# Performance work log

Hardware: AMD Instinct MI355X
Metric: run time of the kernel (lower is better)

The kernel has to match this reference:

```python
import jax, jax.numpy as jnp
import numpy as np

SCALE = 256.0  # emulates SharedFxpShift = 8 fixed-point shift


def requant(x):
    # RequantFxpToScaledInt8: shift down by SharedFxpShift and clamp to int8 range
    return jnp.clip(x / SCALE, -128.0, 127.0)


def prelu(x, a):
    return jnp.where(x >= 0, x, a * x)


def _linearize(c):
    # injective encoding of 3D int coords (coords in [-8, 2040) after +8 shift)
    c = c.astype(jnp.int64) + 8
    B = 2048
    return (c[:, 0] * B + c[:, 1]) * B + c[:, 2]


def sparse_conv(coords, feats, W, stride):
    # 3x3x3 submanifold sparse conv: for each kernel offset, hash-lookup the
    # neighbor via sorted linearized coords + searchsorted, gather, matmul.
    # coords [N,3] int32, feats [N,Cin], W [27,Cin,Cout]
    lin = _linearize(coords)
    perm = jnp.argsort(lin)
    slin = lin[perm]
    N = coords.shape[0]
    out = jnp.zeros((N, W.shape[-1]), feats.dtype)
    k = 0
    for dx in (-1, 0, 1):
        for dy in (-1, 0, 1):
            for dz in (-1, 0, 1):
                off = jnp.array([dx, dy, dz], jnp.int32) * stride
                q = _linearize(coords + off[None, :])
                pos = jnp.clip(jnp.searchsorted(slin, q), 0, N - 1)
                hit = slin[pos] == q
                nb = perm[pos]
                f = jnp.where(hit[:, None], feats[nb], 0.0)
                out = out + f @ W[k]
                k += 1
    return out


def setup_inputs() -> dict:
    N, M, C = 200000, 400000, 64
    rng = np.random.default_rng(0)
    # unique parent coords: multiples of 2 in 512^3 grid
    lin = rng.choice(2 ** 24, size=N, replace=False).astype(np.int64)
    px = (lin // (256 * 256)) % 256
    py = (lin // 256) % 256
    pz = lin % 256
    rec_C = (np.stack([px, py, pz], 1) * 2).astype(np.int32)  # [N,3], stride 2
    # exactly M occupied children out of N*8, sorted (row-major mask order)
    child_idx = np.sort(rng.choice(N * 8, size=M, replace=False)).astype(np.int32)
    parent = child_idx // 8
    bit = child_idx % 8
    off = np.stack([(bit >> 2) & 1, (bit >> 1) & 1, bit & 1], 1).astype(np.int32)
    child_C = rec_C[parent] + off  # [M,3], stride 1, unique
    bins1_bits = np.zeros((N, 8), np.int32)
    bins1_bits[parent, bit] = 1
    bins0_bits = rng.integers(0, 2, size=(M, 8)).astype(np.int32)

    key = jax.random.key(0)
    ks = jax.random.split(key, 20)

    def w(k, shape, fan_in):
        return jax.random.normal(k, shape, jnp.float32) / np.sqrt(fan_in)

    inp = {
        "rec_F": jax.random.normal(ks[0], (N, C), jnp.float32) * SCALE,
        "dec_W": w(ks[1], (C + 8, C), C + 8),
        "dec_b": w(ks[2], (C,), 1) * 0.1,
        "dec_a": jnp.full((C,), 0.25, jnp.float32),
        "res_W1": w(ks[3], (27, C, C), 27 * C),
        "res_b1": w(ks[4], (C,), 1) * 0.1,
        "res_a1": jnp.full((C,), 0.25, jnp.float32),
        "res_W2": w(ks[5], (27, C, C), 27 * C),
        "res_b2": w(ks[6], (C,), 1) * 0.1,
        "p0_Wc": w(ks[7], (27, C, C), 27 * C),
        "p0_bc": w(ks[8], (C,), 1) * 0.1,
        "p0_ac": jnp.full((C,), 0.25, jnp.float32),
        "p0_Wl": w(ks[9], (C, C * 8), C),
        "p1_Wc": w(ks[10], (27, C, C), 27 * C),
        "p1_bc": w(ks[11], (C,), 1) * 0.1,
        "p1_ac": jnp.full((C,), 0.25, jnp.float32),
        "p1_Wl": w(ks[12], (C, 255), C),
        "rec_C": jnp.asarray(rec_C),
        "bins1_bits": jnp.asarray(bins1_bits),
        "child_idx": jnp.asarray(child_idx),
        "child_C": jnp.asarray(child_C),
        "bins0_bits": jnp.asarray(bins0_bits),
    }
    return inp


def reference(rec_F, dec_W, dec_b, dec_a, res_W1, res_b1, res_a1, res_W2, res_b2,
              p0_Wc, p0_bc, p0_ac, p0_Wl, p1_Wc, p1_bc, p1_ac, p1_Wl,
              rec_C, bins1_bits, child_idx, child_C, bins0_bits):
    C = dec_W.shape[1]
    # embed (empty Sequential for pred_steps=2): bins1.F << SharedFxpShift
    embed_f = bins1_bits.astype(jnp.float32) * SCALE  # [N,8]
    x = jnp.concatenate([rec_F, embed_f], 1)  # [N, C+8]
    # dec: Requant -> LinearPReLU(C+8 -> C, out32) -> ResBlock(C)
    h = requant(x)
    h = prelu(h @ dec_W + dec_b, dec_a)  # [N,C]
    r = requant(h)
    r = prelu(sparse_conv(rec_C, r, res_W1, 2) + res_b1, res_a1)
    r = requant(r)
    r = sparse_conv(rec_C, r, res_W2, 2) + res_b2
    rec_out = h + r  # [N,C]
    # pred[0]: Requant -> SparseConvPReLU(out8) -> Linear(C -> 8C, out32)
    p = requant(rec_out)
    p = requant(prelu(sparse_conv(rec_C, p, p0_Wc, 2) + p0_bc, p0_ac))
    p = p @ p0_Wl  # [N, 8C]
    # boolean-mask gather of occupied children: reshape [N,8,C] then mask ->
    # equals flat row gather with precomputed sorted child indices
    p = p.reshape(-1, C)[child_idx]  # [M,C]
    # pred[1] (last): Requant -> SparseConvPReLU(out8) -> Linear(C -> 255, out32)
    p = requant(p)
    p = requant(prelu(sparse_conv(child_C, p, p1_Wc, 1) + p1_bc, p1_ac))
    pred_out = p @ p1_Wl  # [M,255]
    # cur_oct = (cur_bins[0].F << bin2oct_kernel).sum(1) - 1
    k = jnp.arange(8, dtype=jnp.int32)
    cur_oct = ((bins0_bits << k).sum(1) - 1).astype(jnp.int16)  # [M]
    return rec_out, pred_out, cur_oct
```

## Files before the change

### kernel.cpp

```cpp
#include <hip/hip_runtime.h>
#include <stdint.h>


typedef short bf16x8 __attribute__((ext_vector_type(8)));
typedef float f32x4 __attribute__((ext_vector_type(4)));

#define EMPTY_KEY 0xFFFFFFFFu

__device__ __forceinline__ float rq(float x) {
  x *= (1.0f / 256.0f);
  return fminf(fmaxf(x, -128.0f), 127.0f);
}

__device__ __forceinline__ short f2b(float f) {
  union { float f; uint32_t u; } v; v.f = f;
  uint32_t u = v.u;
  uint32_t r = (u + 0x7FFFu + ((u >> 16) & 1u)) >> 16;
  return (short)r;
}

__device__ __forceinline__ uint32_t hkey(int x, int y, int z) {
  return ((uint32_t)(x + 8) << 20) | ((uint32_t)(y + 8) << 10) | (uint32_t)(z + 8);
}
__device__ __forceinline__ uint32_t hfun(uint32_t key, uint32_t mask) {
  return (key * 2654435761u) & mask;
}


__device__ __forceinline__ void pack_conv_elem(const float* __restrict__ W,
                                               short* __restrict__ dst, int gid) {
  int lane = gid & 63;
  int c = (gid >> 6) & 3;
  int t = (gid >> 8) & 1;
  int k = gid >> 9;
  int n = c * 16 + (lane & 15);
  int g = lane >> 4;
  bf16x8 v;
#pragma unroll
  for (int e = 0; e < 8; e++) {
    int kk = t * 32 + g * 8 + e;
    v[e] = f2b(W[(k * 64 + kk) * 64 + n]);
  }
  *(bf16x8*)(dst + gid * 8) = v;
}

__device__ __forceinline__ void pack_dense_elem(const float* __restrict__ W,
                                                short* __restrict__ dst, int K,
                                                int Ncols, int KT, int CT, int gid) {
  if (gid >= KT * CT * 64) return;
  int lane = gid & 63;
  int c = (gid >> 6) % CT;
  int t = gid / (64 * CT);
  int n = c * 16 + (lane & 15);
  int g = lane >> 4;
  bf16x8 v;
#pragma unroll
  for (int e = 0; e < 8; e++) {
    int kk = t * 32 + g * 8 + e;
    float val = (kk < K && n < Ncols) ? W[kk * Ncols + n] : 0.0f;
    v[e] = f2b(val);
  }
  *(bf16x8*)(dst + gid * 8) = v;
}

struct SetupA {
  const float *dec_W, *p0_Wl, *p1_Wl, *res_W1, *res_W2, *p0_Wc, *p1_Wc;
  const int *bins1, *child_idx, *bins0;
  uint32_t* rkeys;
  short *wpack, *decwp, *p0wp, *p1wp;
  int *bitsPk, *pStart, *bcnt;
  float* outOct;
  int N, M;
};

__global__ void __launch_bounds__(256) k_setupA(SetupA s) {
  int bid = blockIdx.x, tid = threadIdx.x;
  if (bid < 2048) {
    s.rkeys[bid * 256 + tid] = EMPTY_KEY;
    return;
  }
  bid -= 2048;
  if (bid < 216) {
    int which = bid / 54, sb = bid % 54;
    int gid = sb * 256 + tid;
    if (gid < 27 * 2 * 4 * 64) {
      const float* W = which == 0 ? s.res_W1 : which == 1 ? s.res_W2
                     : which == 2 ? s.p0_Wc : s.p1_Wc;
      pack_conv_elem(W, s.wpack + which * 110592, gid);
    }
    return;
  }
  bid -= 216;
  if (bid < 27) {
    if (bid < 3) pack_dense_elem(s.dec_W, s.decwp, 72, 64, 3, 4, bid * 256 + tid);
    else if (bid < 19) pack_dense_elem(s.p0_Wl, s.p0wp, 64, 512, 2, 32, (bid - 3) * 256 + tid);
    else pack_dense_elem(s.p1_Wl, s.p1wp, 64, 255, 2, 16, (bid - 19) * 256 + tid);
    return;
  }
  bid -= 27;
  int nbN = (s.N + 255) / 256, nbM = (s.M + 255) / 256;
  if (bid < nbN) {
    int p = bid * 256 + tid;
    if (p < s.N) {
      int b = 0;
#pragma unroll
      for (int e = 0; e < 8; e++) b |= (s.bins1[(size_t)p * 8 + e] & 1) << e;
      s.bitsPk[p] = b;
    }
    return;
  }
  bid -= nbN;
  if (bid < nbM) {
    int m = bid * 256 + tid;
    if (m < s.M) {
      int p = s.child_idx[m] >> 3;
      if (m == 0 || (s.child_idx[m - 1] >> 3) != p) s.pStart[p] = m;
    }
    return;
  }
  bid -= nbM;
  if (bid < nbM) {
    int m = bid * 256 + tid;
    if (m < s.M) {
      int ss = 0;
#pragma unroll
      for (int e = 0; e < 8; e++) ss += s.bins0[(size_t)m * 8 + e] << e;
      s.outOct[m] = (float)(ss - 1);
    }
    return;
  }
  if (tid < 8) s.bcnt[tid] = 0;
}

__global__ void __launch_bounds__(256)
k_setupB(const int* __restrict__ rec_C, const int* __restrict__ child_idx,
         uint32_t* __restrict__ rkeys, int* __restrict__ rvals,
         int* __restrict__ lists, int* __restrict__ cnt, int N, int M) {
  int bid = blockIdx.x, tid = threadIdx.x;
  int nbN = (N + 255) / 256;
  if (bid < nbN) {
    int i = bid * 256 + tid;
    if (i >= N) return;
    uint32_t key = hkey(rec_C[i * 3], rec_C[i * 3 + 1], rec_C[i * 3 + 2]);
    uint32_t s = hfun(key, (1u << 19) - 1);
    while (true) {
      uint32_t old = atomicCAS(&rkeys[s], EMPTY_KEY, key);
      if (old == EMPTY_KEY) { rvals[s] = i; return; }
      s = (s + 1) & ((1u << 19) - 1);
    }
  }
  bid -= nbN;
  __shared__ int lcnt[8];
  __shared__ int lbase[8];
  if (tid < 8) lcnt[tid] = 0;
  __syncthreads();
  int m = bid * 256 + tid;
  int b = 0, lp = 0;
  if (m < M) {
    b = child_idx[m] & 7;
    lp = atomicAdd(&lcnt[b], 1);
  }
  __syncthreads();
  if (tid < 8) lbase[tid] = atomicAdd(&cnt[tid], lcnt[tid]);
  __syncthreads();
  if (m < M) lists[(size_t)b * M + lbase[b] + lp] = m;
}

__global__ void __launch_bounds__(256)
k_setupC1(const int* __restrict__ rec_C,
          const uint32_t* __restrict__ rkeys, const int* __restrict__ rvals,
          int* __restrict__ nbrR, int N) {
  const uint32_t rmask = (1u << 19) - 1;
  int t = blockIdx.x * 256 + threadIdx.x;
  if (t >= N * 27) return;
  int i = t / 27, k = t % 27;
  int dx = k / 9 - 1, dy = (k / 3) % 3 - 1, dz = k % 3 - 1;
  int x = rec_C[i * 3] + dx * 2;
  int y = rec_C[i * 3 + 1] + dy * 2;
  int z = rec_C[i * 3 + 2] + dz * 2;
  uint32_t key = hkey(x, y, z);
  uint32_t s = hfun(key, rmask);
  int res = -1;
  while (true) {
    uint32_t kk = rkeys[s];
    if (kk == key) { res = rvals[s]; break; }
    if (kk == EMPTY_KEY) break;
    s = (s + 1) & rmask;
  }
  nbrR[(size_t)i * 28 + k] = res;
}

__global__ void __launch_bounds__(256)
k_setupC2(const int* __restrict__ child_C, const int* __restrict__ child_idx,
          const int* __restrict__ nbrR, const int* __restrict__ bitsPacked,
          const int* __restrict__ parentStart, int* __restrict__ nbrC, int M) {
  int m = blockIdx.x * 256 + threadIdx.x;
  if (m >= M) return;
  int cx = child_C[(size_t)m * 3], cy = child_C[(size_t)m * 3 + 1],
      cz = child_C[(size_t)m * 3 + 2];
  int pr = child_idx[m] >> 3;
  const int* nrow = nbrR + (size_t)pr * 28;
  int px = cx & 1, py = cy & 1, pz = cz & 1;

  int b8[8], s8[8];
#pragma unroll
  for (int j = 0; j < 8; j++) {
    int ddx = (px - 1) + ((j >> 2) & 1);
    int ddy = (py - 1) + ((j >> 1) & 1);
    int ddz = (pz - 1) + (j & 1);
    int kk = (ddx + 1) * 9 + (ddy + 1) * 3 + (ddz + 1);
    int r = nrow[kk];
    b8[j] = (r >= 0) ? bitsPacked[r] : 0;
    s8[j] = (r >= 0) ? parentStart[r] : 0;
  }

  int nout[28];
  nout[27] = -1;
#pragma unroll
  for (int k = 0; k < 27; k++) {
    const int dx = k / 9 - 1, dy = (k / 3) % 3 - 1, dz = k % 3 - 1;
    int tx = cx + dx, ty = cy + dy, tz = cz + dz;
    int jx = ((px + dx + 2) >> 1) - px;
    int jy = ((py + dy + 2) >> 1) - py;
    int jz = ((pz + dz + 2) >> 1) - pz;
    int j = jx * 4 + jy * 2 + jz;
    int bit = ((tx & 1) << 2) | ((ty & 1) << 1) | (tz & 1);
    int bits = b8[j];
    int res = -1;
    if ((bits >> bit) & 1) res = s8[j] + __popc(bits & ((1 << bit) - 1));
    nout[k] = res;
  }
#pragma unroll
  for (int q = 0; q < 7; q++)
    *(int4*)(nbrC + (size_t)m * 28 + q * 4) =
        make_int4(nout[q * 4], nout[q * 4 + 1], nout[q * 4 + 2], nout[q * 4 + 3]);
}


__global__ void __launch_bounds__(256)
k_dec(const float* __restrict__ recF, const int* __restrict__ bits,
      const short* __restrict__ wp, const float* __restrict__ bias,
      const float* __restrict__ alpha, float* __restrict__ h32,
      short* __restrict__ hq) {
  int tid = threadIdx.x, wid = tid >> 6, lane = tid & 63;
  int rowbase = blockIdx.x * 64 + wid * 16;
  int lrow = rowbase + (lane & 15);
  int g = lane >> 4;
  f32x4 acc[4] = {};
#pragma unroll
  for (int t = 0; t < 3; t++) {
    bf16x8 a = {0, 0, 0, 0, 0, 0, 0, 0};
    if (t < 2) {
      const float* src = recF + (size_t)lrow * 64 + t * 32 + g * 8;
#pragma unroll
      for (int e = 0; e < 8; e++) a[e] = f2b(rq(src[e]));
    } else if (g == 0) {
      const int* bp = bits + (size_t)lrow * 8;
#pragma unroll
      for (int e = 0; e < 8; e++) a[e] = f2b((float)bp[e]);
    }
#pragma unroll
    for (int c = 0; c < 4; c++) {
      bf16x8 b = *(const bf16x8*)(wp + ((t * 4 + c) * 64 + lane) * 8);
      acc[c] = __builtin_amdgcn_mfma_f32_16x16x32_bf16(a, b, acc[c], 0, 0, 0);
    }
  }
#pragma unroll
  for (int c = 0; c < 4; c++) {
    int col = c * 16 + (lane & 15);
    float bi = bias[col], al = alpha[col];
#pragma unroll
    for (int r = 0; r < 4; r++) {
      int row = rowbase + g * 4 + r;
      float v = acc[c][r] + bi;
      v = v >= 0.0f ? v : al * v;
      h32[(size_t)row * 64 + col] = v;
      hq[(size_t)row * 64 + col] = f2b(rq(v));
    }
  }
}

template <int MODE>
__global__ void __launch_bounds__(256)
k_conv(const short* __restrict__ fin, const int* __restrict__ nbr,
       const short* __restrict__ wp, const float* __restrict__ bias,
       const float* __restrict__ alpha, const float* __restrict__ resid,
       float* __restrict__ out32, short* __restrict__ outq) {
  int tid = threadIdx.x, wid = tid >> 6, lane = tid & 63;
  int rowbase = blockIdx.x * 64 + wid * 16;
  int lrow = rowbase + (lane & 15);
  int g = lane >> 4;

  int4 nv[7];
#pragma unroll
  for (int j = 0; j < 7; j++)
    nv[j] = *(const int4*)(nbr + (size_t)lrow * 28 + j * 4);
  int nbk[28];
#pragma unroll
  for (int j = 0; j < 7; j++) {
    nbk[j * 4 + 0] = nv[j].x;
    nbk[j * 4 + 1] = nv[j].y;
    nbk[j * 4 + 2] = nv[j].z;
    nbk[j * 4 + 3] = nv[j].w;
  }

  const bf16x8 zz = {0, 0, 0, 0, 0, 0, 0, 0};
  f32x4 acc[4] = {};
#pragma unroll
  for (int k = 0; k < 27; k++) {
    if (__any(nbk[k] >= 0)) {
      int nb = nbk[k];
      int safe = nb >= 0 ? nb : 0;
      const short* fp = fin + (size_t)safe * 64 + g * 8;
      bf16x8 a0 = *(const bf16x8*)fp;
      bf16x8 a1 = *(const bf16x8*)(fp + 32);
      a0 = nb >= 0 ? a0 : zz;
      a1 = nb >= 0 ? a1 : zz;
      const short* wk = wp + k * 4096;
#pragma unroll
      for (int c = 0; c < 4; c++) {
        bf16x8 b0 = *(const bf16x8*)(wk + (c * 64 + lane) * 8);
        acc[c] = __builtin_amdgcn_mfma_f32_16x16x32_bf16(a0, b0, acc[c], 0, 0, 0);
      }
#pragma unroll
      for (int c = 0; c < 4; c++) {
        bf16x8 b1 = *(const bf16x8*)(wk + ((4 + c) * 64 + lane) * 8);
        acc[c] = __builtin_amdgcn_mfma_f32_16x16x32_bf16(a1, b1, acc[c], 0, 0, 0);
      }
    }
  }
#pragma unroll
  for (int c = 0; c < 4; c++) {
    int col = c * 16 + (lane & 15);
    float bi = bias[col];
    float al = (MODE == 0) ? alpha[col] : 0.0f;
#pragma unroll
    for (int r = 0; r < 4; r++) {
      int row = rowbase + g * 4 + r;
      float v = acc[c][r] + bi;
      if (MODE == 0) {
        v = v >= 0.0f ? v : al * v;
        outq[(size_t)row * 64 + col] = f2b(rq(v));
      } else {
        v += resid[(size_t)row * 64 + col];
        out32[(size_t)row * 64 + col] = v;
        outq[(size_t)row * 64 + col] = f2b(rq(v));
      }
    }
  }
}

__global__ void __launch_bounds__(256)
k_p0(const short* __restrict__ qq, const int* __restrict__ child_idx,
     const int* __restrict__ lists, const int* __restrict__ cnt,
     const short* __restrict__ wp, short* __restrict__ tq, int M) {
  int b = blockIdx.y;
  int cb = cnt[b];
  int start = blockIdx.x * 64;
  if (start >= cb) return;
  int tid = threadIdx.x, wid = tid >> 6, lane = tid & 63, g = lane >> 4;
  int posA = start + wid * 16 + (lane & 15);
  int parent = -1;
  if (posA < cb) parent = child_idx[lists[(size_t)b * M + posA]] >> 3;
  f32x4 acc[4] = {};
#pragma unroll
  for (int t = 0; t < 2; t++) {
    bf16x8 a = {0, 0, 0, 0, 0, 0, 0, 0};
    if (parent >= 0) a = *(const bf16x8*)(qq + (size_t)parent * 64 + t * 32 + g * 8);
#pragma unroll
    for (int c = 0; c < 4; c++) {
      bf16x8 bb = *(const bf16x8*)(wp + (((size_t)t * 32 + b * 4 + c) * 64 + lane) * 8);
      acc[c] = __builtin_amdgcn_mfma_f32_16x16x32_bf16(a, bb, acc[c], 0, 0, 0);
    }
  }
#pragma unroll
  for (int r = 0; r < 4; r++) {
    int posD = start + wid * 16 + g * 4 + r;
    if (posD < cb) {
      int m = lists[(size_t)b * M + posD];
#pragma unroll
      for (int c = 0; c < 4; c++) {
        int col = c * 16 + (lane & 15);
        tq[(size_t)m * 64 + col] = f2b(rq(acc[c][r]));
      }
    }
  }
}

__global__ void __launch_bounds__(256, 4)
k_convp1(const short* __restrict__ fin, const int* __restrict__ nbr,
         const short* __restrict__ wp, const float* __restrict__ bias,
         const float* __restrict__ alpha,
         const int* __restrict__ lists, const int* __restrict__ cnt,
         const short* __restrict__ p1wp, float* __restrict__ out, int M) {
  __shared__ short lds[4][16][64];
  __shared__ int mrow[4][16];
  int tid = threadIdx.x, wid = tid >> 6, lane = tid & 63;
  int l15 = lane & 15, g = lane >> 4;

  int pos = blockIdx.x * 64 + wid * 16 + l15;
  int m = -1;
  if (pos < M) {
    int rem = pos, b = 0;
#pragma unroll
    for (int i = 0; i < 7; i++) {
      int ci = cnt[i];
      if (b == i && rem >= ci) { rem -= ci; b = i + 1; }
    }
    m = lists[(size_t)b * M + rem];
  }
  if (g == 0) mrow[wid][l15] = m;

  int4 nv[7];
#pragma unroll
  for (int j = 0; j < 7; j++) {
    if (m >= 0) nv[j] = *(const int4*)(nbr + (size_t)m * 28 + j * 4);
    else nv[j] = make_int4(-1, -1, -1, -1);
  }
  int nbk[28];
#pragma unroll
  for (int j = 0; j < 7; j++) {
    nbk[j * 4 + 0] = nv[j].x;
    nbk[j * 4 + 1] = nv[j].y;
    nbk[j * 4 + 2] = nv[j].z;
    nbk[j * 4 + 3] = nv[j].w;
  }

  const bf16x8 zz = {0, 0, 0, 0, 0, 0, 0, 0};
  f32x4 acc[4] = {};
#pragma unroll
  for (int k = 0; k < 27; k++) {
    if (__any(nbk[k] >= 0)) {
      int nb = nbk[k];
      int safe = nb >= 0 ? nb : 0;
      const short* fp = fin + (size_t)safe * 64 + g * 8;
      bf16x8 a0 = *(const bf16x8*)fp;
      bf16x8 a1 = *(const bf16x8*)(fp + 32);
      a0 = nb >= 0 ? a0 : zz;
      a1 = nb >= 0 ? a1 : zz;
      const short* wk = wp + k * 4096;
#pragma unroll
      for (int c = 0; c < 4; c++) {
        bf16x8 b0 = *(const bf16x8*)(wk + (c * 64 + lane) * 8);
        acc[c] = __builtin_amdgcn_mfma_f32_16x16x32_bf16(a0, b0, acc[c], 0, 0, 0);
      }
#pragma unroll
      for (int c = 0; c < 4; c++) {
        bf16x8 b1 = *(const bf16x8*)(wk + ((4 + c) * 64 + lane) * 8);
        acc[c] = __builtin_amdgcn_mfma_f32_16x16x32_bf16(a1, b1, acc[c], 0, 0, 0);
      }
    }
  }

#pragma unroll
  for (int c = 0; c < 4; c++) {
    int col = c * 16 + l15;
    float bi = bias[col], al = alpha[col];
#pragma unroll
    for (int r = 0; r < 4; r++) {
      int rowW = g * 4 + r;
      float v = acc[c][r] + bi;
      v = v >= 0.0f ? v : al * v;
      lds[wid][rowW][col ^ ((rowW & 7) << 3)] = f2b(rq(v));
    }
  }
  __syncthreads();

  bf16x8 a0 = *(const bf16x8*)&lds[wid][l15][(g * 8) ^ ((l15 & 7) << 3)];
  bf16x8 a1 = *(const bf16x8*)&lds[wid][l15][(32 + g * 8) ^ ((l15 & 7) << 3)];
#pragma unroll
  for (int grp = 0; grp < 4; grp++) {
    f32x4 a2[4] = {};
#pragma unroll
    for (int c = 0; c < 4; c++) {
      bf16x8 b0 = *(const bf16x8*)(p1wp + ((grp * 4 + c) * 64 + lane) * 8);
      a2[c] = __builtin_amdgcn_mfma_f32_16x16x32_bf16(a0, b0, a2[c], 0, 0, 0);
      bf16x8 b1 = *(const bf16x8*)(p1wp + ((16 + grp * 4 + c) * 64 + lane) * 8);
      a2[c] = __builtin_amdgcn_mfma_f32_16x16x32_bf16(a1, b1, a2[c], 0, 0, 0);
    }
#pragma unroll
    for (int r = 0; r < 4; r++) {
      int mo = mrow[wid][g * 4 + r];
      if (mo >= 0) {
#pragma unroll
        for (int c = 0; c < 4; c++) {
          int col = (grp * 4 + c) * 16 + l15;
          if (col < 255) out[(size_t)mo * 255 + col] = a2[c][r];
        }
      }
    }
  }
}


extern "C" void kernel_launch(void* const* d_in, const int* in_sizes, int n_in,
                              void* d_out, int out_size, void* d_ws, size_t ws_size,
                              hipStream_t stream) {
  const float* rec_F  = (const float*)d_in[0];
  const float* dec_W  = (const float*)d_in[1];
  const float* dec_b  = (const float*)d_in[2];
  const float* dec_a  = (const float*)d_in[3];
  const float* res_W1 = (const float*)d_in[4];
  const float* res_b1 = (const float*)d_in[5];
  const float* res_a1 = (const float*)d_in[6];
  const float* res_W2 = (const float*)d_in[7];
  const float* res_b2 = (const float*)d_in[8];
  const float* p0_Wc  = (const float*)d_in[9];
  const float* p0_bc  = (const float*)d_in[10];
  const float* p0_ac  = (const float*)d_in[11];
  const float* p0_Wl  = (const float*)d_in[12];
  const float* p1_Wc  = (const float*)d_in[13];
  const float* p1_bc  = (const float*)d_in[14];
  const float* p1_ac  = (const float*)d_in[15];
  const float* p1_Wl  = (const float*)d_in[16];
  const int* rec_C    = (const int*)d_in[17];
  const int* bins1    = (const int*)d_in[18];
  const int* child_idx= (const int*)d_in[19];
  const int* child_C  = (const int*)d_in[20];
  const int* bins0    = (const int*)d_in[21];

  const int N = in_sizes[0] / 64;
  const int M = in_sizes[19];

  char* ws = (char*)d_ws;
  size_t off = 0;
  auto alloc = [&](size_t bytes) -> char* {
    char* p = ws + off;
    off += (bytes + 255) & ~(size_t)255;
    return p;
  };
  const uint32_t HR = 1u << 19;
  uint32_t* rkeys = (uint32_t*)alloc((size_t)HR * 4);
  int*      rvals = (int*)alloc((size_t)HR * 4);
  int* nbrR = (int*)alloc((size_t)N * 28 * 4);
  int* nbrC = (int*)alloc((size_t)M * 28 * 4);
  short* wpack = (short*)alloc((size_t)4 * 110592 * 2);
  short* decwp = (short*)alloc((size_t)3 * 4 * 64 * 8 * 2);
  short* p0wp  = (short*)alloc((size_t)2 * 32 * 64 * 8 * 2);
  short* p1wp  = (short*)alloc((size_t)2 * 16 * 64 * 8 * 2);
  short* bufA = (short*)alloc((size_t)N * 64 * 2);
  short* bufB = (short*)alloc((size_t)N * 64 * 2);
  float* h32  = (float*)alloc((size_t)N * 64 * 4);
  short* tq   = (short*)alloc((size_t)M * 64 * 2);
  int* lists  = (int*)alloc((size_t)8 * M * 4);
  int* bcnt   = (int*)alloc(256);
  int* bitsPk = (int*)alloc((size_t)N * 4);
  int* pStart = (int*)alloc((size_t)N * 4);

  float* outRec  = (float*)d_out;
  float* outPred = outRec + (size_t)N * 64;
  float* outOct  = outPred + (size_t)M * 255;

  dim3 B(256);
  int nbN = (N + 255) / 256, nbM = (M + 255) / 256;

  SetupA sa = {dec_W, p0_Wl, p1_Wl, res_W1, res_W2, p0_Wc, p1_Wc,
               bins1, child_idx, bins0, rkeys, wpack, decwp, p0wp, p1wp,
               bitsPk, pStart, bcnt, outOct, N, M};
  int gridA = 2048 + 216 + 27 + nbN + nbM + nbM + 1;
  k_setupA<<<gridA, B, 0, stream>>>(sa);
  k_setupB<<<nbN + nbM, B, 0, stream>>>(rec_C, child_idx, rkeys, rvals,
                                        lists, bcnt, N, M);
  k_setupC1<<<(N * 27 + 255) / 256, B, 0, stream>>>(rec_C, rkeys, rvals, nbrR, N);
  k_setupC2<<<nbM, B, 0, stream>>>(child_C, child_idx, nbrR, bitsPk, pStart,
                                   nbrC, M);

  k_dec<<<N / 64, B, 0, stream>>>(rec_F, bins1, decwp, dec_b, dec_a, h32, bufA);
  k_conv<0><<<N / 64, B, 0, stream>>>(bufA, nbrR, wpack, res_b1, res_a1,
                                      nullptr, nullptr, bufB);
  k_conv<1><<<N / 64, B, 0, stream>>>(bufB, nbrR, wpack + 110592, res_b2, nullptr,
                                      h32, outRec, bufA);
  k_conv<0><<<N / 64, B, 0, stream>>>(bufA, nbrR, wpack + 221184, p0_bc, p0_ac,
                                      nullptr, nullptr, bufB);
  k_p0<<<dim3(M / 64, 8), B, 0, stream>>>(bufB, child_idx, lists, bcnt, p0wp, tq, M);
  k_convp1<<<(M + 63) / 64, B, 0, stream>>>(tq, nbrC, wpack + 331776, p1_bc, p1_ac,
                                            lists, bcnt, p1wp, outPred, M);
}
```

Before: 618.3 us.

## Split convp1 grid by child bit and prefetch sibling neighbor features upfront

Launches the last sparse conv with a 2D grid where blockIdx.y selects the child-bit bucket, so each block reads from a single list and skips the per-thread bucket search. Because all children in a bucket share the same offset within their parent, the 8 kernel offsets that can land on siblings in the same parent are known ahead of time. Their features are loaded up front in one batch for memory-level parallelism, and those offsets are then skipped in the data-dependent 27-offset loop. This adds register pressure from 16 held bf16x8 vectors and launches 8x as many blocks, most of which exit early.

```diff
diff --git a/kernel.cpp b/kernel.cpp
--- a/kernel.cpp
+++ b/kernel.cpp
@@ -395,42 +395,79 @@
          const short* __restrict__ p1wp, float* __restrict__ out, int M) {
   __shared__ short lds[4][16][64];
   __shared__ int mrow[4][16];
+  int b = blockIdx.y;
+  int cb = cnt[b];
+  int start = blockIdx.x * 64;
+  if (start >= cb) return;
   int tid = threadIdx.x, wid = tid >> 6, lane = tid & 63;
   int l15 = lane & 15, g = lane >> 4;
 
-  int pos = blockIdx.x * 64 + wid * 16 + l15;
-  int m = -1;
-  if (pos < M) {
-    int rem = pos, b = 0;
-#pragma unroll
-    for (int i = 0; i < 7; i++) {
-      int ci = cnt[i];
-      if (b == i && rem >= ci) { rem -= ci; b = i + 1; }
-    }
-    m = lists[(size_t)b * M + rem];
-  }
+  int pos = start + wid * 16 + l15;
+  int m = (pos < cb) ? lists[(size_t)b * M + pos] : -1;
   if (g == 0) mrow[wid][l15] = m;
 
+  int msafe = m >= 0 ? m : 0;
+  const int* nrow = nbr + (size_t)msafe * 28;
+
+  int px = (b >> 2) & 1, py = (b >> 1) & 1, pz = b & 1;
+  int kown[8];
+  uint32_t ownMask = 0;
+#pragma unroll
+  for (int j = 0; j < 8; j++) {
+    int k = (((j >> 2) & 1) - px + 1) * 9 + (((j >> 1) & 1) - py + 1) * 3 +
+            ((j & 1) - pz + 1);
+    kown[j] = k;
+    ownMask |= 1u << k;
+  }
+
+  int nbo[8];
+#pragma unroll
+  for (int j = 0; j < 8; j++) nbo[j] = nrow[kown[j]];
   int4 nv[7];
 #pragma unroll
+  for (int j = 0; j < 7; j++) nv[j] = *(const int4*)(nrow + j * 4);
+
+  const bf16x8 zz = {0, 0, 0, 0, 0, 0, 0, 0};
+
+  bf16x8 A0[8], A1[8];
+#pragma unroll
+  for (int j = 0; j < 8; j++) {
+    int nb = (m >= 0) ? nbo[j] : -1;
+    int safe = nb >= 0 ? nb : 0;
+    const short* fp = fin + (size_t)safe * 64 + g * 8;
+    bf16x8 x0 = *(const bf16x8*)fp;
+    bf16x8 x1 = *(const bf16x8*)(fp + 32);
+    A0[j] = nb >= 0 ? x0 : zz;
+    A1[j] = nb >= 0 ? x1 : zz;
+  }
+
+  f32x4 acc[4] = {};
+#pragma unroll
+  for (int j = 0; j < 8; j++) {
+    const short* wk = wp + kown[j] * 4096;
+#pragma unroll
+    for (int c = 0; c < 4; c++) {
+      bf16x8 b0 = *(const bf16x8*)(wk + (c * 64 + lane) * 8);
+      acc[c] = __builtin_amdgcn_mfma_f32_16x16x32_bf16(A0[j], b0, acc[c], 0, 0, 0);
+    }
+#pragma unroll
+    for (int c = 0; c < 4; c++) {
+      bf16x8 b1 = *(const bf16x8*)(wk + ((4 + c) * 64 + lane) * 8);
+      acc[c] = __builtin_amdgcn_mfma_f32_16x16x32_bf16(A1[j], b1, acc[c], 0, 0, 0);
+    }
+  }
+
+  int nbk[28];
+#pragma unroll
   for (int j = 0; j < 7; j++) {
-    if (m >= 0) nv[j] = *(const int4*)(nbr + (size_t)m * 28 + j * 4);
-    else nv[j] = make_int4(-1, -1, -1, -1);
-  }
-  int nbk[28];
-#pragma unroll
-  for (int j = 0; j < 7; j++) {
-    nbk[j * 4 + 0] = nv[j].x;
-    nbk[j * 4 + 1] = nv[j].y;
-    nbk[j * 4 + 2] = nv[j].z;
-    nbk[j * 4 + 3] = nv[j].w;
-  }
-
-  const bf16x8 zz = {0, 0, 0, 0, 0, 0, 0, 0};
-  f32x4 acc[4] = {};
+    nbk[j * 4 + 0] = m >= 0 ? nv[j].x : -1;
+    nbk[j * 4 + 1] = m >= 0 ? nv[j].y : -1;
+    nbk[j * 4 + 2] = m >= 0 ? nv[j].z : -1;
+    nbk[j * 4 + 3] = m >= 0 ? nv[j].w : -1;
+  }
 #pragma unroll
   for (int k = 0; k < 27; k++) {
-    if (__any(nbk[k] >= 0)) {
+    if (!((ownMask >> k) & 1) && __any(nbk[k] >= 0)) {
       int nb = nbk[k];
       int safe = nb >= 0 ? nb : 0;
       const short* fp = fin + (size_t)safe * 64 + g * 8;
@@ -573,6 +610,6 @@
   k_conv<0><<<N / 64, B, 0, stream>>>(bufA, nbrR, wpack + 221184, p0_bc, p0_ac,
                                       nullptr, nullptr, bufB);
   k_p0<<<dim3(M / 64, 8), B, 0, stream>>>(bufB, child_idx, lists, bcnt, p0wp, tq, M);
-  k_convp1<<<(M + 63) / 64, B, 0, stream>>>(tq, nbrC, wpack + 331776, p1_bc, p1_ac,
-                                            lists, bcnt, p1wp, outPred, M);
-}
+  k_convp1<<<dim3((M + 63) / 64, 8), B, 0, stream>>>(
+      tq, nbrC, wpack + 331776, p1_bc, p1_ac, lists, bcnt, p1wp, outPred, M);
+}
```

Result: no change. 620.6 us (+0.4%).

## Split fused p1 conv+linear into sequential-row conv and separate linear kernel

Applied to the files above, without the earlier changes.

The fused p1 kernel, which walked rows in occupancy-bucket order through a list indirection, is replaced by two kernels. One is the generic conv kernel run over child rows in natural order, always computing all 27 offsets with no warp-level skip, writing an int8-requantized bf16 intermediate. The other is a separate linear kernel with coalesced row-ordered output writes. This trades an extra M×64 bf16 round trip through memory and a kernel launch for coalesced stores and simpler control flow. Launch bounds on k_conv are also raised to four blocks per CU.

```diff
diff --git a/kernel.cpp b/kernel.cpp
--- a/kernel.cpp
+++ b/kernel.cpp
@@ -280,8 +280,8 @@
   }
 }
 
-template <int MODE>
-__global__ void __launch_bounds__(256)
+template <int MODE, bool SKIP>
+__global__ void __launch_bounds__(256, 4)
 k_conv(const short* __restrict__ fin, const int* __restrict__ nbr,
        const short* __restrict__ wp, const float* __restrict__ bias,
        const float* __restrict__ alpha, const float* __restrict__ resid,
@@ -308,7 +308,7 @@
   f32x4 acc[4] = {};
 #pragma unroll
   for (int k = 0; k < 27; k++) {
-    if (__any(nbk[k] >= 0)) {
+    if (!SKIP || __any(nbk[k] >= 0)) {
       int nb = nbk[k];
       int safe = nb >= 0 ? nb : 0;
       const short* fp = fin + (size_t)safe * 64 + g * 8;
@@ -388,86 +388,14 @@
 }
 
 __global__ void __launch_bounds__(256, 4)
-k_convp1(const short* __restrict__ fin, const int* __restrict__ nbr,
-         const short* __restrict__ wp, const float* __restrict__ bias,
-         const float* __restrict__ alpha,
-         const int* __restrict__ lists, const int* __restrict__ cnt,
-         const short* __restrict__ p1wp, float* __restrict__ out, int M) {
-  __shared__ short lds[4][16][64];
-  __shared__ int mrow[4][16];
+k_p1(const short* __restrict__ uq, const short* __restrict__ p1wp,
+     float* __restrict__ out) {
   int tid = threadIdx.x, wid = tid >> 6, lane = tid & 63;
   int l15 = lane & 15, g = lane >> 4;
-
-  int pos = blockIdx.x * 64 + wid * 16 + l15;
-  int m = -1;
-  if (pos < M) {
-    int rem = pos, b = 0;
-#pragma unroll
-    for (int i = 0; i < 7; i++) {
-      int ci = cnt[i];
-      if (b == i && rem >= ci) { rem -= ci; b = i + 1; }
-    }
-    m = lists[(size_t)b * M + rem];
-  }
-  if (g == 0) mrow[wid][l15] = m;
-
-  int4 nv[7];
-#pragma unroll
-  for (int j = 0; j < 7; j++) {
-    if (m >= 0) nv[j] = *(const int4*)(nbr + (size_t)m * 28 + j * 4);
-    else nv[j] = make_int4(-1, -1, -1, -1);
-  }
-  int nbk[28];
-#pragma unroll
-  for (int j = 0; j < 7; j++) {
-    nbk[j * 4 + 0] = nv[j].x;
-    nbk[j * 4 + 1] = nv[j].y;
-    nbk[j * 4 + 2] = nv[j].z;
-    nbk[j * 4 + 3] = nv[j].w;
-  }
-
-  const bf16x8 zz = {0, 0, 0, 0, 0, 0, 0, 0};
-  f32x4 acc[4] = {};
-#pragma unroll
-  for (int k = 0; k < 27; k++) {
-    if (__any(nbk[k] >= 0)) {
-      int nb = nbk[k];
-      int safe = nb >= 0 ? nb : 0;
-      const short* fp = fin + (size_t)safe * 64 + g * 8;
-      bf16x8 a0 = *(const bf16x8*)fp;
-      bf16x8 a1 = *(const bf16x8*)(fp + 32);
-      a0 = nb >= 0 ? a0 : zz;
-      a1 = nb >= 0 ? a1 : zz;
-      const short* wk = wp + k * 4096;
-#pragma unroll
-      for (int c = 0; c < 4; c++) {
-        bf16x8 b0 = *(const bf16x8*)(wk + (c * 64 + lane) * 8);
-        acc[c] = __builtin_amdgcn_mfma_f32_16x16x32_bf16(a0, b0, acc[c], 0, 0, 0);
-      }
-#pragma unroll
-      for (int c = 0; c < 4; c++) {
-        bf16x8 b1 = *(const bf16x8*)(wk + ((4 + c) * 64 + lane) * 8);
-        acc[c] = __builtin_amdgcn_mfma_f32_16x16x32_bf16(a1, b1, acc[c], 0, 0, 0);
-      }
-    }
-  }
-
-#pragma unroll
-  for (int c = 0; c < 4; c++) {
-    int col = c * 16 + l15;
-    float bi = bias[col], al = alpha[col];
-#pragma unroll
-    for (int r = 0; r < 4; r++) {
-      int rowW = g * 4 + r;
-      float v = acc[c][r] + bi;
-      v = v >= 0.0f ? v : al * v;
-      lds[wid][rowW][col ^ ((rowW & 7) << 3)] = f2b(rq(v));
-    }
-  }
-  __syncthreads();
-
-  bf16x8 a0 = *(const bf16x8*)&lds[wid][l15][(g * 8) ^ ((l15 & 7) << 3)];
-  bf16x8 a1 = *(const bf16x8*)&lds[wid][l15][(32 + g * 8) ^ ((l15 & 7) << 3)];
+  int rowbase = blockIdx.x * 64 + wid * 16;
+  int lrow = rowbase + l15;
+  bf16x8 a0 = *(const bf16x8*)(uq + (size_t)lrow * 64 + g * 8);
+  bf16x8 a1 = *(const bf16x8*)(uq + (size_t)lrow * 64 + 32 + g * 8);
 #pragma unroll
   for (int grp = 0; grp < 4; grp++) {
     f32x4 a2[4] = {};
@@ -480,13 +408,11 @@
     }
 #pragma unroll
     for (int r = 0; r < 4; r++) {
-      int mo = mrow[wid][g * 4 + r];
-      if (mo >= 0) {
-#pragma unroll
-        for (int c = 0; c < 4; c++) {
-          int col = (grp * 4 + c) * 16 + l15;
-          if (col < 255) out[(size_t)mo * 255 + col] = a2[c][r];
-        }
+      int row = rowbase + g * 4 + r;
+#pragma unroll
+      for (int c = 0; c < 4; c++) {
+        int col = (grp * 4 + c) * 16 + l15;
+        if (col < 255) out[(size_t)row * 255 + col] = a2[c][r];
       }
     }
   }
@@ -542,6 +468,7 @@
   short* bufB = (short*)alloc((size_t)N * 64 * 2);
   float* h32  = (float*)alloc((size_t)N * 64 * 4);
   short* tq   = (short*)alloc((size_t)M * 64 * 2);
+  short* uq   = (short*)alloc((size_t)M * 64 * 2);
   int* lists  = (int*)alloc((size_t)8 * M * 4);
   int* bcnt   = (int*)alloc(256);
   int* bitsPk = (int*)alloc((size_t)N * 4);
@@ -566,13 +493,14 @@
                                    nbrC, M);
 
   k_dec<<<N / 64, B, 0, stream>>>(rec_F, bins1, decwp, dec_b, dec_a, h32, bufA);
-  k_conv<0><<<N / 64, B, 0, stream>>>(bufA, nbrR, wpack, res_b1, res_a1,
-                                      nullptr, nullptr, bufB);
-  k_conv<1><<<N / 64, B, 0, stream>>>(bufB, nbrR, wpack + 110592, res_b2, nullptr,
-                                      h32, outRec, bufA);
-  k_conv<0><<<N / 64, B, 0, stream>>>(bufA, nbrR, wpack + 221184, p0_bc, p0_ac,
-                                      nullptr, nullptr, bufB);
+  k_conv<0, true><<<N / 64, B, 0, stream>>>(bufA, nbrR, wpack, res_b1, res_a1,
+                                            nullptr, nullptr, bufB);
+  k_conv<1, true><<<N / 64, B, 0, stream>>>(bufB, nbrR, wpack + 110592, res_b2,
+                                            nullptr, h32, outRec, bufA);
+  k_conv<0, true><<<N / 64, B, 0, stream>>>(bufA, nbrR, wpack + 221184, p0_bc,
+                                            p0_ac, nullptr, nullptr, bufB);
   k_p0<<<dim3(M / 64, 8), B, 0, stream>>>(bufB, child_idx, lists, bcnt, p0wp, tq, M);
-  k_convp1<<<(M + 63) / 64, B, 0, stream>>>(tq, nbrC, wpack + 331776, p1_bc, p1_ac,
-                                            lists, bcnt, p1wp, outPred, M);
-}
+  k_conv<0, false><<<M / 64, B, 0, stream>>>(tq, nbrC, wpack + 331776, p1_bc,
+                                             p1_ac, nullptr, nullptr, uq);
+  k_p1<<<M / 64, B, 0, stream>>>(uq, p1wp, outPred);
+}
```

Measured after the change: 706.4 us. 14.2% more time.
